# Performance work log

Hardware: AMD Instinct MI355X
Metric: run time of the kernel (lower is better)

The kernel has to match this reference:

```python
import jax, jax.numpy as jnp
import numpy as np

N, IN_C, HID, OUT_C = 50000, 128, 256, 40
L, G = 4, 2
GC = HID // G  # 128 channels per group
E = 600000
EPS = 1e-5


def _ln(h, g, b):
    mu = jnp.mean(h, axis=-1, keepdims=True)
    var = jnp.mean((h - mu) ** 2, axis=-1, keepdims=True)
    return (h - mu) * jax.lax.rsqrt(var + EPS) * g + b


def setup_inputs() -> dict:
    key = jax.random.key(0)
    ks = jax.random.split(key, 16)
    s = lambda k, shape, sc=0.05: jax.random.normal(k, shape, dtype=jnp.float32) * sc
    return {
        "x": jax.random.normal(ks[0], (N, IN_C), dtype=jnp.float32),
        "edge_index": jax.random.randint(ks[1], (2, E), 0, N, dtype=jnp.int64),
        "edge_weight": jax.random.uniform(ks[2], (E,), dtype=jnp.float32),
        "lin1_w": s(ks[3], (IN_C, HID)),
        "lin1_b": jnp.zeros((HID,), jnp.float32),
        "lin2_w": s(ks[4], (HID, OUT_C)),
        "lin2_b": jnp.zeros((OUT_C,), jnp.float32),
        "norm_g": jnp.ones((L, G, GC), jnp.float32),   # per-block LayerNorm gamma
        "norm_b": jnp.zeros((L, G, GC), jnp.float32),  # per-block LayerNorm beta
        "conv_w": s(ks[5], (L, G, GC, GC)),            # per-block GCNConv weight
        "conv_b": jnp.zeros((L, G, GC), jnp.float32),  # per-block GCNConv bias
        "fnorm_g": jnp.ones((HID,), jnp.float32),
        "fnorm_b": jnp.zeros((HID,), jnp.float32),
    }


def reference(x, edge_index, edge_weight, lin1_w, lin1_b, lin2_w, lin2_b,
              norm_g, norm_b, conv_w, conv_b, fnorm_g, fnorm_b):
    src, dst = edge_index[0], edge_index[1]
    h = x @ lin1_w + lin1_b  # [N, HID]
    for l in range(L):
        xs = jnp.split(h, G, axis=-1)  # G x [N, GC]
        ys = []
        y_in = xs[-1]  # GroupAddRev coupling: y_i = x_i + F_i(y_{i-1}), y_{-1} = x_{G-1}
        for g in range(G):
            # GNNBlock: LayerNorm -> ReLU -> GCNConv(normalize=False)
            z = jax.nn.relu(_ln(y_in, norm_g[l, g], norm_b[l, g]))
            z = z @ conv_w[l, g]                       # GCNConv linear
            msg = edge_weight[:, None] * z[src]        # [E, GC]
            agg = jax.ops.segment_sum(msg, dst, num_segments=N) + conv_b[l, g]
            y_in = xs[g] + agg
            ys.append(y_in)
        h = jnp.concatenate(ys, axis=-1)
    h = jax.nn.relu(_ln(h, fnorm_g, fnorm_b))
    return h @ lin2_w + lin2_b  # [N, OUT_C]
```

## Files before the change

### kernel.cpp

```cpp
#include <hip/hip_runtime.h>
#include <stdint.h>

#define NN    50000
#define INC   128
#define HIDC  256
#define OUTC  40
#define GCH   128
#define NL    4
#define NG    2
#define NEDGE 600000
#define EPSV  1e-5f

typedef __bf16 bf16x8 __attribute__((ext_vector_type(8)));
typedef float  f32x4  __attribute__((ext_vector_type(4)));
typedef unsigned short u16x4 __attribute__((ext_vector_type(4)));
typedef unsigned short u16x8 __attribute__((ext_vector_type(8)));

__device__ __forceinline__ float bf2f(unsigned short u) {
    union { float f; unsigned int i; } v;
    v.i = ((unsigned int)u) << 16;
    return v.f;
}
__device__ __forceinline__ unsigned short f2bf(float f) {
    union { float f; unsigned int i; } v;
    v.f = f;
    unsigned int u = v.i;
    u += 0x7FFFu + ((u >> 16) & 1u);
    return (unsigned short)(u >> 16);
}
__device__ __forceinline__ float ldf(const void* p, int is_f32, long long i) {
    if (is_f32) return ((const float*)p)[i];
    return bf2f(((const unsigned short*)p)[i]);
}
__device__ __forceinline__ void gload_lds16(const void* g, void* l) {
    __builtin_amdgcn_global_load_lds(
        (const __attribute__((address_space(1))) unsigned int*)g,
        (__attribute__((address_space(3))) unsigned int*)l,
        16, 0, 0);
}

__global__ void k_marker(void* out, float val, int n) {
    int i = blockIdx.x * 256 + threadIdx.x;
    if (i < n) ((unsigned short*)out)[i] = f2bf(val);
}

__global__ void k_detect(const int* ei, const unsigned short* xprobe,
                         int* flags, int* deg) {
    int t = threadIdx.x;
    int gid = blockIdx.x * 256 + t;
    if (gid < NN) deg[gid] = 0;
    if (blockIdx.x == 0) {
        __shared__ int hi_or, wild_cnt;
        if (t == 0) { hi_or = 0; wild_cnt = 0; }
        __syncthreads();
        int acc = 0;
        for (int i = 0; i < 8; i++) acc |= ei[2 * (t + i * 256) + 1];
        if (acc) atomicOr(&hi_or, 1);
        int wild = 0;
        for (int i = 0; i < 2; i++) {
            unsigned short u = xprobe[t + i * 256];
            int e = (u >> 7) & 0xFF;
            if (e <= 0x30 || e >= 0xC0) wild++;
        }
        atomicAdd(&wild_cnt, wild);
        __syncthreads();
        if (t == 0) {
            flags[0] = hi_or ? 0 : 1;
            flags[1] = (wild_cnt > 32) ? 1 : 0;
        }
    }
}

#define CVT_W1  32768
#define CVT_CW  131072
#define CVT_W2  12288
#define CVT_TOT (CVT_W1 + CVT_CW + CVT_W2)

__global__ void k_convert(const void* w1, const void* cw, const void* w2,
                          const void* b1, const void* ng, const void* nb, const void* cb,
                          const void* fg, const void* fb, const void* b2,
                          const int* flags,
                          unsigned short* w1t, unsigned short* cwt, unsigned short* w2t,
                          float* b1f, float* ngf, float* nbf, float* cbf,
                          float* fgf, float* fbf, float* b2f) {
    int t = threadIdx.x;
    int f32 = flags[1];
    if (blockIdx.x == gridDim.x - 1) {
        b1f[t] = ldf(b1, f32, t);
        fgf[t] = ldf(fg, f32, t);
        fbf[t] = ldf(fb, f32, t);
        if (t < 48) b2f[t] = (t < OUTC) ? ldf(b2, f32, t) : 0.0f;
        for (int i = 0; i < 4; i++) {
            int j = t + i * 256;
            ngf[j] = ldf(ng, f32, j);
            nbf[j] = ldf(nb, f32, j);
            cbf[j] = ldf(cb, f32, j);
        }
        return;
    }
    long long j = (long long)blockIdx.x * 256 + t;
    if (j >= CVT_TOT) return;
    if (j < CVT_W1) {
        int n = (int)(j >> 7), k = (int)(j & 127);
        w1t[n * 128 + (k ^ ((n & 7) << 3))] = f2bf(ldf(w1, f32, (long long)k * HIDC + n));
    } else if (j < CVT_W1 + CVT_CW) {
        long long jj = j - CVT_W1;
        int lg = (int)(jj >> 14);
        int rem = (int)(jj & 16383);
        int n = rem >> 7, k = rem & 127;
        cwt[lg * 16384 + n * 128 + (k ^ ((n & 7) << 3))] =
            f2bf(ldf(cw, f32, (long long)lg * GCH * GCH + (long long)k * GCH + n));
    } else {
        long long jj = j - (CVT_W1 + CVT_CW);
        int n = (int)(jj >> 8), k = (int)(jj & 255);
        w2t[n * 256 + (k ^ ((n & 7) << 3))] =
            (n < OUTC) ? f2bf(ldf(w2, f32, (long long)k * OUTC + n)) : (unsigned short)0;
    }
}

__global__ void k_count(const int* __restrict__ ei, const int* __restrict__ flags,
                        int* __restrict__ deg) {
    int e = (blockIdx.x * 256 + threadIdx.x) * 2;
    if (e >= NEDGE) return;
    int d0, d1;
    if (flags[0]) {
        int4 v = *(const int4*)(ei + 2 * (NEDGE + e));
        d0 = v.x; d1 = v.z;
    } else {
        int2 v = *(const int2*)(ei + NEDGE + e);
        d0 = v.x; d1 = v.y;
    }
    atomicAdd(&deg[d0], 1);
    if (e + 1 < NEDGE) atomicAdd(&deg[d1], 1);
}

#define SCAN_B 49
__global__ void k_scan_a(const int* __restrict__ deg, int* __restrict__ bsum) {
    __shared__ int part[256];
    int b = blockIdx.x, t = threadIdx.x;
    int base = b * 1024 + t * 4;
    int s = 0;
#pragma unroll
    for (int j = 0; j < 4; j++) {
        int i = base + j;
        if (i < NN) s += deg[i];
    }
    part[t] = s;
    __syncthreads();
    for (int off = 128; off > 0; off >>= 1) {
        if (t < off) part[t] += part[t + off];
        __syncthreads();
    }
    if (t == 0) bsum[b] = part[0];
}

__global__ void k_scan_c(const int* __restrict__ deg, const int* __restrict__ bsum,
                         int* __restrict__ rowptr, int* __restrict__ cursor) {
    __shared__ int part[256];
    __shared__ int bbase;
    int b = blockIdx.x, t = threadIdx.x;
    if (t == 0) { int r = 0; for (int i = 0; i < b; i++) r += bsum[i]; bbase = r; }
    int base = b * 1024 + t * 4;
    int v[4];
    int s = 0;
#pragma unroll
    for (int j = 0; j < 4; j++) {
        int i = base + j;
        v[j] = (i < NN) ? deg[i] : 0;
        s += v[j];
    }
    part[t] = s;
    __syncthreads();
    for (int off = 1; off < 256; off <<= 1) {
        int x = (t >= off) ? part[t - off] : 0;
        __syncthreads();
        part[t] += x;
        __syncthreads();
    }
    int run = bbase + part[t] - s;
#pragma unroll
    for (int j = 0; j < 4; j++) {
        int i = base + j;
        if (i < NN) { rowptr[i] = run; cursor[i] = run; }
        run += v[j];
    }
    if (b == SCAN_B - 1 && t == 255) rowptr[NN] = NEDGE;
}

__global__ void k_fill(const int* __restrict__ ei, const void* __restrict__ ew,
                       const int* __restrict__ flags,
                       int* __restrict__ cursor, unsigned int* __restrict__ epk) {
    int e = (blockIdx.x * 256 + threadIdx.x) * 2;
    if (e >= NEDGE) return;
    int is64 = flags[0];
    int f32 = flags[1];
    int d0, s0, d1 = 0, s1 = 0;
    int has1 = (e + 1 < NEDGE);
    if (is64) {
        d0 = ei[2 * (NEDGE + e)];
        s0 = ei[2 * e];
        if (has1) { d1 = ei[2 * (NEDGE + e) + 2]; s1 = ei[2 * e + 2]; }
    } else {
        d0 = ei[NEDGE + e];
        s0 = ei[e];
        if (has1) { d1 = ei[NEDGE + e + 1]; s1 = ei[e + 1]; }
    }
    int p0 = atomicAdd(&cursor[d0], 1);
    int p1 = has1 ? atomicAdd(&cursor[d1], 1) : 0;
    unsigned int w0 = f2bf(ldf(ew, f32, e));
    epk[p0] = (w0 << 16) | (unsigned int)s0;
    if (has1) {
        unsigned int w1 = f2bf(ldf(ew, f32, e + 1));
        epk[p1] = (w1 << 16) | (unsigned int)s1;
    }
}

__global__ __launch_bounds__(256) void k_first(
    const void* __restrict__ x,
    const unsigned short* __restrict__ w1t,
    const float* __restrict__ b1f,
    const float* __restrict__ ngf, const float* __restrict__ nbf,
    const unsigned short* __restrict__ cw0,
    const int* __restrict__ flags,
    unsigned short* __restrict__ h,
    unsigned short* __restrict__ z0)
{
    __shared__ __align__(16) unsigned short xb[64 * 128];
    __shared__ __align__(16) unsigned short wt[128 * 128];
    int t = threadIdx.x;
    int r0 = blockIdx.x * 64;
    int f32x = flags[1];
    int w = t >> 6, lane = t & 63, quad = lane >> 4, ln = lane & 15;
    const f32x4 zf = {0.f, 0.f, 0.f, 0.f};

#pragma unroll
    for (int i = 0; i < 8; i++) {
        int cb = (i * 256 + t) * 16;
        gload_lds16((const char*)w1t + cb, (char*)wt + cb);
    }
#pragma unroll
    for (int i = 0; i < 4; i++) {
        int chunk = i * 256 + t;
        int row = chunk >> 4, c16 = chunk & 15;
        int grow = r0 + row;
        u16x8 val = {0, 0, 0, 0, 0, 0, 0, 0};
        if (grow < NN) {
            if (f32x) {
                const float* p = (const float*)x + (long long)grow * INC + c16 * 8;
                float4 a = *(const float4*)p;
                float4 c = *(const float4*)(p + 4);
                val[0] = f2bf(a.x); val[1] = f2bf(a.y); val[2] = f2bf(a.z); val[3] = f2bf(a.w);
                val[4] = f2bf(c.x); val[5] = f2bf(c.y); val[6] = f2bf(c.z); val[7] = f2bf(c.w);
            } else {
                val = *(const u16x8*)((const unsigned short*)x + (long long)grow * INC + c16 * 8);
            }
        }
        *(u16x8*)((char*)xb + row * 256 + ((c16 * 16) ^ ((row & 7) << 4))) = val;
    }
    __syncthreads();

    f32x4 acc[2][8];
#pragma unroll
    for (int i = 0; i < 2; i++)
#pragma unroll
        for (int j = 0; j < 8; j++) acc[i][j] = zf;

#pragma unroll
    for (int kk = 0; kk < 4; kk++) {
        int cb = kk * 64 + quad * 16;
        int rA = w * 16 + ln;
        bf16x8 a = *(const bf16x8*)((const char*)xb + rA * 256 + (cb ^ ((rA & 7) << 4)));
#pragma unroll
        for (int nf = 0; nf < 8; nf++) {
            int rB = nf * 16 + ln;
            bf16x8 b = *(const bf16x8*)((const char*)wt + rB * 256 + (cb ^ ((rB & 7) << 4)));
            acc[0][nf] = __builtin_amdgcn_mfma_f32_16x16x32_bf16(a, b, acc[0][nf], 0, 0, 0);
        }
    }
    __syncthreads();
#pragma unroll
    for (int i = 0; i < 8; i++) {
        int cb = (i * 256 + t) * 16;
        gload_lds16((const char*)w1t + 32768 + cb, (char*)wt + cb);
    }
    __syncthreads();
#pragma unroll
    for (int kk = 0; kk < 4; kk++) {
        int cb = kk * 64 + quad * 16;
        int rA = w * 16 + ln;
        bf16x8 a = *(const bf16x8*)((const char*)xb + rA * 256 + (cb ^ ((rA & 7) << 4)));
#pragma unroll
        for (int nf = 0; nf < 8; nf++) {
            int rB = nf * 16 + ln;
            bf16x8 b = *(const bf16x8*)((const char*)wt + rB * 256 + (cb ^ ((rB & 7) << 4)));
            acc[1][nf] = __builtin_amdgcn_mfma_f32_16x16x32_bf16(a, b, acc[1][nf], 0, 0, 0);
        }
    }

    float ga8[8], be8[8], yv[8][4];
#pragma unroll
    for (int nf = 0; nf < 8; nf++) {
        int col = nf * 16 + ln;
        float b0 = b1f[col], b1 = b1f[128 + col];
        ga8[nf] = ngf[col]; be8[nf] = nbf[col];
#pragma unroll
        for (int r4 = 0; r4 < 4; r4++) {
            int row = r0 + w * 16 + quad * 4 + r4;
            unsigned short h0 = f2bf(acc[0][nf][r4] + b0);
            unsigned short h1 = f2bf(acc[1][nf][r4] + b1);
            if (row < NN) {
                h[(long long)row * HIDC + col] = h0;
                h[(long long)row * HIDC + 128 + col] = h1;
            }
            yv[nf][r4] = bf2f(h1);
        }
    }
    __syncthreads();
#pragma unroll
    for (int i = 0; i < 8; i++) {
        int cb = (i * 256 + t) * 16;
        gload_lds16((const char*)cw0 + cb, (char*)wt + cb);
    }
    unsigned short* a_tile = xb;
#pragma unroll
    for (int r4 = 0; r4 < 4; r4++) {
        float s = 0.f, q = 0.f;
#pragma unroll
        for (int nf = 0; nf < 8; nf++) { s += yv[nf][r4]; q += yv[nf][r4] * yv[nf][r4]; }
        s += __shfl_xor(s, 1, 64); s += __shfl_xor(s, 2, 64);
        s += __shfl_xor(s, 4, 64); s += __shfl_xor(s, 8, 64);
        q += __shfl_xor(q, 1, 64); q += __shfl_xor(q, 2, 64);
        q += __shfl_xor(q, 4, 64); q += __shfl_xor(q, 8, 64);
        float mu = s * (1.0f / GCH);
        float var = q * (1.0f / GCH) - mu * mu;
        float rs = rsqrtf(var + EPSV);
        int row = w * 16 + quad * 4 + r4;
#pragma unroll
        for (int nf = 0; nf < 8; nf++) {
            float val = (yv[nf][r4] - mu) * rs * ga8[nf] + be8[nf];
            if (val < 0.f) val = 0.f;
            *(unsigned short*)((char*)a_tile + row * 256 +
                               (((nf * 16 + ln) * 2) ^ ((row & 7) << 4))) = f2bf(val);
        }
    }
    __syncthreads();

    f32x4 acc2[8];
#pragma unroll
    for (int j = 0; j < 8; j++) acc2[j] = zf;
#pragma unroll
    for (int kk = 0; kk < 4; kk++) {
        int cb = kk * 64 + quad * 16;
        int rA = w * 16 + ln;
        bf16x8 a = *(const bf16x8*)((const char*)a_tile + rA * 256 + (cb ^ ((rA & 7) << 4)));
#pragma unroll
        for (int nf = 0; nf < 8; nf++) {
            int rB = nf * 16 + ln;
            bf16x8 b = *(const bf16x8*)((const char*)wt + rB * 256 + (cb ^ ((rB & 7) << 4)));
            acc2[nf] = __builtin_amdgcn_mfma_f32_16x16x32_bf16(a, b, acc2[nf], 0, 0, 0);
        }
    }
#pragma unroll
    for (int nf = 0; nf < 8; nf++) {
        int col = nf * 16 + ln;
#pragma unroll
        for (int r4 = 0; r4 < 4; r4++) {
            int row2 = r0 + w * 16 + quad * 4 + r4;
            if (row2 < NN) z0[(long long)row2 * GCH + col] = f2bf(acc2[nf][r4]);
        }
    }
}

__global__ __launch_bounds__(256) void k_fused(
    const int* __restrict__ rowptr, const unsigned int* __restrict__ epk,
    const unsigned short* __restrict__ zin,
    const float* __restrict__ cb,
    unsigned short* __restrict__ h, int out_half,
    const float* __restrict__ ga, const float* __restrict__ be,
    const unsigned short* __restrict__ cwn,
    unsigned short* __restrict__ zout)
{
    __shared__ __align__(16) unsigned short wt[128 * 128];
    __shared__ __align__(16) unsigned short a_tile[64 * 128];
    int t = threadIdx.x;
    int r0 = blockIdx.x * 64;
    int c8 = (t & 15) << 3;

#pragma unroll
    for (int i = 0; i < 8; i++) {
        int cbyte = (i * 256 + t) * 16;
        gload_lds16((const char*)cwn + cbyte, (char*)wt + cbyte);
    }

#pragma unroll 1
    for (int bt = 0; bt < 4; bt++) {
        int row = bt * 16 + (t >> 4);
        int node = r0 + row;
        if (node < NN) {
            int beg = rowptr[node], end = rowptr[node + 1];
            unsigned short* hp = h + (long long)node * HIDC + out_half * GCH + c8;
            u16x8 hv = *(u16x8*)hp;
            const unsigned short* zb = zin + c8;
            float acc[8];
#pragma unroll
            for (int j = 0; j < 8; j++) acc[j] = 0.f;

            int e = beg;
            for (; e + 7 < end; e += 8) {
                unsigned int pe[8];
                u16x8 v[8];
#pragma unroll
                for (int i = 0; i < 8; i++) pe[i] = epk[e + i];
#pragma unroll
                for (int i = 0; i < 8; i++)
                    v[i] = *(const u16x8*)(zb + (long long)(pe[i] & 0xFFFFu) * GCH);
#pragma unroll
                for (int i = 0; i < 8; i++) {
                    float wv = bf2f((unsigned short)(pe[i] >> 16));
#pragma unroll
                    for (int j = 0; j < 8; j++) acc[j] += wv * bf2f(v[i][j]);
                }
            }
            if (e + 3 < end) {
                unsigned int pe[4];
                u16x8 v[4];
#pragma unroll
                for (int i = 0; i < 4; i++) pe[i] = epk[e + i];
#pragma unroll
                for (int i = 0; i < 4; i++)
                    v[i] = *(const u16x8*)(zb + (long long)(pe[i] & 0xFFFFu) * GCH);
#pragma unroll
                for (int i = 0; i < 4; i++) {
                    float wv = bf2f((unsigned short)(pe[i] >> 16));
#pragma unroll
                    for (int j = 0; j < 8; j++) acc[j] += wv * bf2f(v[i][j]);
                }
                e += 4;
            }
            for (; e < end; e++) {
                unsigned int pe = epk[e];
                float w0 = bf2f((unsigned short)(pe >> 16));
                u16x8 v = *(const u16x8*)(zb + (long long)(pe & 0xFFFFu) * GCH);
#pragma unroll
                for (int j = 0; j < 8; j++) acc[j] += w0 * bf2f(v[j]);
            }

            float y[8]; float sum = 0.f, sq = 0.f;
#pragma unroll
            for (int j = 0; j < 8; j++) {
                float yy = bf2f(hv[j]) + acc[j] + cb[c8 + j];
                unsigned short r = f2bf(yy);
                hv[j] = r;
                y[j] = bf2f(r);
                sum += y[j]; sq += y[j] * y[j];
            }
            *(u16x8*)hp = hv;

            sum += __shfl_xor(sum, 1, 64); sum += __shfl_xor(sum, 2, 64);
            sum += __shfl_xor(sum, 4, 64); sum += __shfl_xor(sum, 8, 64);
            sq  += __shfl_xor(sq, 1, 64);  sq  += __shfl_xor(sq, 2, 64);
            sq  += __shfl_xor(sq, 4, 64);  sq  += __shfl_xor(sq, 8, 64);
            float mu = sum * (1.0f / GCH);
            float var = sq * (1.0f / GCH) - mu * mu;
            float rs = rsqrtf(var + EPSV);
            u16x8 o;
#pragma unroll
            for (int j = 0; j < 8; j++) {
                float val = (y[j] - mu) * rs * ga[c8 + j] + be[c8 + j];
                if (val < 0.f) val = 0.f;
                o[j] = f2bf(val);
            }
            *(u16x8*)((char*)a_tile + row * 256 + ((c8 * 2) ^ ((row & 7) << 4))) = o;
        }
    }
    __syncthreads();

    int w = t >> 6, lane = t & 63, quad = lane >> 4, ln = lane & 15;
    const f32x4 zf = {0.f, 0.f, 0.f, 0.f};
    f32x4 acc2[8];
#pragma unroll
    for (int j = 0; j < 8; j++) acc2[j] = zf;
#pragma unroll
    for (int kk = 0; kk < 4; kk++) {
        int cbyte = kk * 64 + quad * 16;
        int rA = w * 16 + ln;
        bf16x8 a = *(const bf16x8*)((const char*)a_tile + rA * 256 + (cbyte ^ ((rA & 7) << 4)));
#pragma unroll
        for (int nf = 0; nf < 8; nf++) {
            int rB = nf * 16 + ln;
            bf16x8 b = *(const bf16x8*)((const char*)wt + rB * 256 + (cbyte ^ ((rB & 7) << 4)));
            acc2[nf] = __builtin_amdgcn_mfma_f32_16x16x32_bf16(a, b, acc2[nf], 0, 0, 0);
        }
    }
#pragma unroll
    for (int nf = 0; nf < 8; nf++) {
        int col = nf * 16 + ln;
#pragma unroll
        for (int r4 = 0; r4 < 4; r4++) {
            int row2 = r0 + w * 16 + quad * 4 + r4;
            if (row2 < NN) zout[(long long)row2 * GCH + col] = f2bf(acc2[nf][r4]);
        }
    }
}

__global__ __launch_bounds__(256) void k_last(
    const int* __restrict__ rowptr, const unsigned int* __restrict__ epk,
    const unsigned short* __restrict__ zin,
    const float* __restrict__ cb,
    unsigned short* __restrict__ h,
    const float* __restrict__ fgf, const float* __restrict__ fbf,
    const unsigned short* __restrict__ w2t,
    const float* __restrict__ b2f,
    const int* __restrict__ flags,
    void* __restrict__ out)
{
    __shared__ __align__(16) unsigned short a_tile[64 * 256];
    __shared__ __align__(16) unsigned short wt[48 * 256];
    int t = threadIdx.x;
    int r0 = blockIdx.x * 64;
    int c8 = (t & 15) << 3;
    const int out_half = 1;

#pragma unroll
    for (int i = 0; i < 6; i++) {
        int cbyte = (i * 256 + t) * 16;
        gload_lds16((const char*)w2t + cbyte, (char*)wt + cbyte);
    }

#pragma unroll 1
    for (int bt = 0; bt < 4; bt++) {
        int row = bt * 16 + (t >> 4);
        int node = r0 + row;
        if (node < NN) {
            int beg = rowptr[node], end = rowptr[node + 1];
            unsigned short* hp = h + (long long)node * HIDC + out_half * GCH + c8;
            u16x8 hv = *(u16x8*)hp;
            const unsigned short* zb = zin + c8;
            float acc[8];
#pragma unroll
            for (int j = 0; j < 8; j++) acc[j] = 0.f;

            int e = beg;
            for (; e + 3 < end; e += 4) {
                unsigned int pe[4];
                u16x8 v[4];
#pragma unroll
                for (int i = 0; i < 4; i++) pe[i] = epk[e + i];
#pragma unroll
                for (int i = 0; i < 4; i++)
                    v[i] = *(const u16x8*)(zb + (long long)(pe[i] & 0xFFFFu) * GCH);
#pragma unroll
                for (int i = 0; i < 4; i++) {
                    float wv = bf2f((unsigned short)(pe[i] >> 16));
#pragma unroll
                    for (int j = 0; j < 8; j++) acc[j] += wv * bf2f(v[i][j]);
                }
            }
            for (; e < end; e++) {
                unsigned int pe = epk[e];
                float w0 = bf2f((unsigned short)(pe >> 16));
                u16x8 v = *(const u16x8*)(zb + (long long)(pe & 0xFFFFu) * GCH);
#pragma unroll
                for (int j = 0; j < 8; j++) acc[j] += w0 * bf2f(v[j]);
            }

            float y[8]; float sum = 0.f, sq = 0.f;
#pragma unroll
            for (int j = 0; j < 8; j++) {
                float yy = bf2f(hv[j]) + acc[j] + cb[c8 + j];
                unsigned short r = f2bf(yy);
                hv[j] = r;
                y[j] = bf2f(r);
                sum += y[j]; sq += y[j] * y[j];
            }
            *(u16x8*)hp = hv;

            float oy[8];
            u16x8 ov = *(const u16x8*)(h + (long long)node * HIDC + (out_half ^ 1) * GCH + c8);
#pragma unroll
            for (int j = 0; j < 8; j++) {
                oy[j] = bf2f(ov[j]);
                sum += oy[j]; sq += oy[j] * oy[j];
            }
            sum += __shfl_xor(sum, 1, 64); sum += __shfl_xor(sum, 2, 64);
            sum += __shfl_xor(sum, 4, 64); sum += __shfl_xor(sum, 8, 64);
            sq  += __shfl_xor(sq, 1, 64);  sq  += __shfl_xor(sq, 2, 64);
            sq  += __shfl_xor(sq, 4, 64);  sq  += __shfl_xor(sq, 8, 64);
            float mu = sum * (1.0f / HIDC);
            float var = sq * (1.0f / HIDC) - mu * mu;
            float rs = rsqrtf(var + EPSV);

            u16x8 o;
            int cn = out_half * GCH + c8;
#pragma unroll
            for (int j = 0; j < 8; j++) {
                float val = (y[j] - mu) * rs * fgf[cn + j] + fbf[cn + j];
                if (val < 0.f) val = 0.f;
                o[j] = f2bf(val);
            }
            *(u16x8*)((char*)a_tile + row * 512 + ((cn * 2) ^ ((row & 7) << 4))) = o;
            int co = (out_half ^ 1) * GCH + c8;
#pragma unroll
            for (int j = 0; j < 8; j++) {
                float val = (oy[j] - mu) * rs * fgf[co + j] + fbf[co + j];
                if (val < 0.f) val = 0.f;
                o[j] = f2bf(val);
            }
            *(u16x8*)((char*)a_tile + row * 512 + ((co * 2) ^ ((row & 7) << 4))) = o;
        }
    }
    __syncthreads();

    int w = t >> 6, lane = t & 63, quad = lane >> 4, ln = lane & 15;
    const f32x4 zf = {0.f, 0.f, 0.f, 0.f};
    f32x4 acc2[3];
#pragma unroll
    for (int j = 0; j < 3; j++) acc2[j] = zf;
#pragma unroll
    for (int kk = 0; kk < 8; kk++) {
        int cbyte = kk * 64 + quad * 16;
        int row = w * 16 + ln;
        bf16x8 a = *(const bf16x8*)((const char*)a_tile + row * 512 + (cbyte ^ ((row & 7) << 4)));
#pragma unroll
        for (int nf = 0; nf < 3; nf++) {
            int rB = nf * 16 + ln;
            bf16x8 b = *(const bf16x8*)((const char*)wt + rB * 512 + (cbyte ^ ((rB & 7) << 4)));
            acc2[nf] = __builtin_amdgcn_mfma_f32_16x16x32_bf16(a, b, acc2[nf], 0, 0, 0);
        }
    }
    int f32o = flags[1];
#pragma unroll
    for (int nf = 0; nf < 3; nf++) {
        int col = nf * 16 + ln;
        if (col >= OUTC) continue;
        float bias = b2f[col];
#pragma unroll
        for (int r4 = 0; r4 < 4; r4++) {
            int row2 = r0 + w * 16 + quad * 4 + r4;
            if (row2 < NN) {
                float val = acc2[nf][r4] + bias;
                long long o = (long long)row2 * OUTC + col;
                if (f32o) ((float*)out)[o] = val;
                else      ((unsigned short*)out)[o] = f2bf(val);
            }
        }
    }
}

extern "C" void kernel_launch(void* const* d_in, const int* in_sizes, int n_in,
                              void* d_out, int out_size, void* d_ws, size_t ws_size,
                              hipStream_t stream)
{
    const void* x       = d_in[0];
    const int*  ei      = (const int*)d_in[1];
    const void* ew      = d_in[2];
    const void* lin1_w  = d_in[3];
    const void* lin1_b  = d_in[4];
    const void* lin2_w  = d_in[5];
    const void* lin2_b  = d_in[6];
    const void* norm_g  = d_in[7];
    const void* norm_b  = d_in[8];
    const void* conv_w  = d_in[9];
    const void* conv_b  = d_in[10];
    const void* fnorm_g = d_in[11];
    const void* fnorm_b = d_in[12];

    char* ws = (char*)d_ws;
    size_t off = 0;
    auto alloc = [&](size_t bytes) { void* p = (void*)(ws + off); off += (bytes + 255) & ~255ull; return p; };

    unsigned short* h      = (unsigned short*)alloc((size_t)NN * HIDC * 2);
    unsigned short* z0     = (unsigned short*)alloc((size_t)NN * GCH * 2);
    unsigned short* z1     = (unsigned short*)alloc((size_t)NN * GCH * 2);
    unsigned short* w1t    = (unsigned short*)alloc((size_t)CVT_W1 * 2);
    unsigned short* cwt    = (unsigned short*)alloc((size_t)CVT_CW * 2);
    unsigned short* w2t    = (unsigned short*)alloc((size_t)CVT_W2 * 2);
    float*          b1f    = (float*)alloc(256 * 4);
    float*          ngf    = (float*)alloc(1024 * 4);
    float*          nbf    = (float*)alloc(1024 * 4);
    float*          cbf    = (float*)alloc(1024 * 4);
    float*          fgf    = (float*)alloc(256 * 4);
    float*          fbf    = (float*)alloc(256 * 4);
    float*          b2f    = (float*)alloc(48 * 4);
    int*            deg    = (int*)alloc((size_t)NN * 4);
    int*            rowptr = (int*)alloc(((size_t)NN + 1) * 4);
    int*            cursor = (int*)alloc((size_t)NN * 4);
    unsigned int*   epk    = (unsigned int*)alloc((size_t)NEDGE * 4);
    int*            flags  = (int*)alloc(256);
    int*            bsum   = (int*)alloc(SCAN_B * 4);

    if (ws_size < off || n_in < 13) {
        float mv = 100.0f + (float)(ws_size >> 20) + ((n_in < 13) ? 10000.0f : 0.0f);
        k_marker<<<(out_size + 255) / 256, 256, 0, stream>>>(d_out, mv, out_size);
        return;
    }

    k_detect<<<196, 256, 0, stream>>>(ei, (const unsigned short*)x, flags, deg);
    k_convert<<<CVT_TOT / 256 + 1, 256, 0, stream>>>(lin1_w, conv_w, lin2_w,
                                                     lin1_b, norm_g, norm_b, conv_b,
                                                     fnorm_g, fnorm_b, lin2_b, flags,
                                                     w1t, cwt, w2t,
                                                     b1f, ngf, nbf, cbf, fgf, fbf, b2f);
    k_count<<<(NEDGE / 2 + 255) / 256, 256, 0, stream>>>(ei, flags, deg);
    k_scan_a<<<SCAN_B, 256, 0, stream>>>(deg, bsum);
    k_scan_c<<<SCAN_B, 256, 0, stream>>>(deg, bsum, rowptr, cursor);
    k_fill<<<(NEDGE / 2 + 255) / 256, 256, 0, stream>>>(ei, ew, flags, cursor, epk);

    const int GB = (NN + 63) / 64;
    k_first<<<GB, 256, 0, stream>>>(x, w1t, b1f, ngf, nbf, cwt, flags, h, z0);
    for (int lg = 0; lg < NL * NG - 1; lg++) {
        unsigned short* zin  = (lg & 1) ? z1 : z0;
        unsigned short* zout = (lg & 1) ? z0 : z1;
        k_fused<<<GB, 256, 0, stream>>>(rowptr, epk, zin, cbf + lg * GCH, h, lg & 1,
                                        ngf + (lg + 1) * GCH, nbf + (lg + 1) * GCH,
                                        cwt + (size_t)(lg + 1) * 16384, zout);
    }
    k_last<<<GB, 256, 0, stream>>>(rowptr, epk, z1, cbf + 7 * GCH, h,
                                   fgf, fbf, w2t, b2f, flags, d_out);
}
```

Baseline: 578.7 us.

## Halve weight LDS tiles, stage weights in phases, raise occupancy hints

Shrinks the weight staging buffer in k_first and k_fused to 64x128 and loads weights in quarter or half chunks with extra barriers between phases. Adds launch_bounds minimum of 5 blocks per SM. k_last drops its LDS weight copy and reads W2 directly from global memory, and unrolls the edge gather loop by 8. The smaller LDS footprint is meant to allow more resident blocks to hide gather latency, at the cost of more synchronisation, possible register pressure from the occupancy hint, and uncached global reads of W2.

```diff
diff --git a/kernel.cpp b/kernel.cpp
--- a/kernel.cpp
+++ b/kernel.cpp
@@ -31,6 +31,9 @@
 __device__ __forceinline__ float ldf(const void* p, int is_f32, long long i) {
     if (is_f32) return ((const float*)p)[i];
     return bf2f(((const unsigned short*)p)[i]);
+}
+__device__ __forceinline__ bf16x8 ld8(const unsigned short* p) {
+    return *(const bf16x8*)p;
 }
 __device__ __forceinline__ void gload_lds16(const void* g, void* l) {
     __builtin_amdgcn_global_load_lds(
@@ -215,7 +218,7 @@
     }
 }
 
-__global__ __launch_bounds__(256) void k_first(
+__global__ __launch_bounds__(256, 5) void k_first(
     const void* __restrict__ x,
     const unsigned short* __restrict__ w1t,
     const float* __restrict__ b1f,
@@ -226,7 +229,7 @@
     unsigned short* __restrict__ z0)
 {
     __shared__ __align__(16) unsigned short xb[64 * 128];
-    __shared__ __align__(16) unsigned short wt[128 * 128];
+    __shared__ __align__(16) unsigned short wt[64 * 128];
     int t = threadIdx.x;
     int r0 = blockIdx.x * 64;
     int f32x = flags[1];
@@ -234,7 +237,7 @@
     const f32x4 zf = {0.f, 0.f, 0.f, 0.f};
 
 #pragma unroll
-    for (int i = 0; i < 8; i++) {
+    for (int i = 0; i < 4; i++) {
         int cb = (i * 256 + t) * 16;
         gload_lds16((const char*)w1t + cb, (char*)wt + cb);
     }
@@ -266,35 +269,36 @@
         for (int j = 0; j < 8; j++) acc[i][j] = zf;
 
 #pragma unroll
-    for (int kk = 0; kk < 4; kk++) {
-        int cb = kk * 64 + quad * 16;
-        int rA = w * 16 + ln;
-        bf16x8 a = *(const bf16x8*)((const char*)xb + rA * 256 + (cb ^ ((rA & 7) << 4)));
-#pragma unroll
-        for (int nf = 0; nf < 8; nf++) {
-            int rB = nf * 16 + ln;
-            bf16x8 b = *(const bf16x8*)((const char*)wt + rB * 256 + (cb ^ ((rB & 7) << 4)));
-            acc[0][nf] = __builtin_amdgcn_mfma_f32_16x16x32_bf16(a, b, acc[0][nf], 0, 0, 0);
-        }
-    }
-    __syncthreads();
-#pragma unroll
-    for (int i = 0; i < 8; i++) {
+    for (int ph = 0; ph < 4; ph++) {
+        int nh = ph >> 1, s = ph & 1;
+#pragma unroll
+        for (int kk = 0; kk < 4; kk++) {
+            int cb = kk * 64 + quad * 16;
+            int rA = w * 16 + ln;
+            bf16x8 a = *(const bf16x8*)((const char*)xb + rA * 256 + (cb ^ ((rA & 7) << 4)));
+#pragma unroll
+            for (int nfl = 0; nfl < 4; nfl++) {
+                int rB = nfl * 16 + ln;
+                bf16x8 b = *(const bf16x8*)((const char*)wt + rB * 256 + (cb ^ ((rB & 7) << 4)));
+                acc[nh][s * 4 + nfl] =
+                    __builtin_amdgcn_mfma_f32_16x16x32_bf16(a, b, acc[nh][s * 4 + nfl], 0, 0, 0);
+            }
+        }
+        __syncthreads();
+        if (ph < 3) {
+#pragma unroll
+            for (int i = 0; i < 4; i++) {
+                int cb = (i * 256 + t) * 16;
+                gload_lds16((const char*)w1t + (ph + 1) * 16384 + cb, (char*)wt + cb);
+            }
+            __syncthreads();
+        }
+    }
+
+#pragma unroll
+    for (int i = 0; i < 4; i++) {
         int cb = (i * 256 + t) * 16;
-        gload_lds16((const char*)w1t + 32768 + cb, (char*)wt + cb);
-    }
-    __syncthreads();
-#pragma unroll
-    for (int kk = 0; kk < 4; kk++) {
-        int cb = kk * 64 + quad * 16;
-        int rA = w * 16 + ln;
-        bf16x8 a = *(const bf16x8*)((const char*)xb + rA * 256 + (cb ^ ((rA & 7) << 4)));
-#pragma unroll
-        for (int nf = 0; nf < 8; nf++) {
-            int rB = nf * 16 + ln;
-            bf16x8 b = *(const bf16x8*)((const char*)wt + rB * 256 + (cb ^ ((rB & 7) << 4)));
-            acc[1][nf] = __builtin_amdgcn_mfma_f32_16x16x32_bf16(a, b, acc[1][nf], 0, 0, 0);
-        }
+        gload_lds16((const char*)cw0 + cb, (char*)wt + cb);
     }
 
     float ga8[8], be8[8], yv[8][4];
@@ -314,12 +318,6 @@
             }
             yv[nf][r4] = bf2f(h1);
         }
-    }
-    __syncthreads();
-#pragma unroll
-    for (int i = 0; i < 8; i++) {
-        int cb = (i * 256 + t) * 16;
-        gload_lds16((const char*)cw0 + cb, (char*)wt + cb);
     }
     unsigned short* a_tile = xb;
 #pragma unroll
@@ -349,15 +347,28 @@
 #pragma unroll
     for (int j = 0; j < 8; j++) acc2[j] = zf;
 #pragma unroll
-    for (int kk = 0; kk < 4; kk++) {
-        int cb = kk * 64 + quad * 16;
-        int rA = w * 16 + ln;
-        bf16x8 a = *(const bf16x8*)((const char*)a_tile + rA * 256 + (cb ^ ((rA & 7) << 4)));
-#pragma unroll
-        for (int nf = 0; nf < 8; nf++) {
-            int rB = nf * 16 + ln;
-            bf16x8 b = *(const bf16x8*)((const char*)wt + rB * 256 + (cb ^ ((rB & 7) << 4)));
-            acc2[nf] = __builtin_amdgcn_mfma_f32_16x16x32_bf16(a, b, acc2[nf], 0, 0, 0);
+    for (int s = 0; s < 2; s++) {
+#pragma unroll
+        for (int kk = 0; kk < 4; kk++) {
+            int cb = kk * 64 + quad * 16;
+            int rA = w * 16 + ln;
+            bf16x8 a = *(const bf16x8*)((const char*)a_tile + rA * 256 + (cb ^ ((rA & 7) << 4)));
+#pragma unroll
+            for (int nfl = 0; nfl < 4; nfl++) {
+                int rB = nfl * 16 + ln;
+                bf16x8 b = *(const bf16x8*)((const char*)wt + rB * 256 + (cb ^ ((rB & 7) << 4)));
+                acc2[s * 4 + nfl] =
+                    __builtin_amdgcn_mfma_f32_16x16x32_bf16(a, b, acc2[s * 4 + nfl], 0, 0, 0);
+            }
+        }
+        if (s == 0) {
+            __syncthreads();
+#pragma unroll
+            for (int i = 0; i < 4; i++) {
+                int cb = (i * 256 + t) * 16;
+                gload_lds16((const char*)cw0 + 16384 + cb, (char*)wt + cb);
+            }
+            __syncthreads();
         }
     }
 #pragma unroll
@@ -371,7 +382,7 @@
     }
 }
 
-__global__ __launch_bounds__(256) void k_fused(
+__global__ __launch_bounds__(256, 5) void k_fused(
     const int* __restrict__ rowptr, const unsigned int* __restrict__ epk,
     const unsigned short* __restrict__ zin,
     const float* __restrict__ cb,
@@ -380,14 +391,14 @@
     const unsigned short* __restrict__ cwn,
     unsigned short* __restrict__ zout)
 {
-    __shared__ __align__(16) unsigned short wt[128 * 128];
+    __shared__ __align__(16) unsigned short wt[64 * 128];
     __shared__ __align__(16) unsigned short a_tile[64 * 128];
     int t = threadIdx.x;
     int r0 = blockIdx.x * 64;
     int c8 = (t & 15) << 3;
 
 #pragma unroll
-    for (int i = 0; i < 8; i++) {
+    for (int i = 0; i < 4; i++) {
         int cbyte = (i * 256 + t) * 16;
         gload_lds16((const char*)cwn + cbyte, (char*)wt + cbyte);
     }
@@ -481,15 +492,28 @@
 #pragma unroll
     for (int j = 0; j < 8; j++) acc2[j] = zf;
 #pragma unroll
-    for (int kk = 0; kk < 4; kk++) {
-        int cbyte = kk * 64 + quad * 16;
-        int rA = w * 16 + ln;
-        bf16x8 a = *(const bf16x8*)((const char*)a_tile + rA * 256 + (cbyte ^ ((rA & 7) << 4)));
-#pragma unroll
-        for (int nf = 0; nf < 8; nf++) {
-            int rB = nf * 16 + ln;
-            bf16x8 b = *(const bf16x8*)((const char*)wt + rB * 256 + (cbyte ^ ((rB & 7) << 4)));
-            acc2[nf] = __builtin_amdgcn_mfma_f32_16x16x32_bf16(a, b, acc2[nf], 0, 0, 0);
+    for (int s = 0; s < 2; s++) {
+#pragma unroll
+        for (int kk = 0; kk < 4; kk++) {
+            int cbyte = kk * 64 + quad * 16;
+            int rA = w * 16 + ln;
+            bf16x8 a = *(const bf16x8*)((const char*)a_tile + rA * 256 + (cbyte ^ ((rA & 7) << 4)));
+#pragma unroll
+            for (int nfl = 0; nfl < 4; nfl++) {
+                int rB = nfl * 16 + ln;
+                bf16x8 b = *(const bf16x8*)((const char*)wt + rB * 256 + (cbyte ^ ((rB & 7) << 4)));
+                acc2[s * 4 + nfl] =
+                    __builtin_amdgcn_mfma_f32_16x16x32_bf16(a, b, acc2[s * 4 + nfl], 0, 0, 0);
+            }
+        }
+        if (s == 0) {
+            __syncthreads();
+#pragma unroll
+            for (int i = 0; i < 4; i++) {
+                int cbyte = (i * 256 + t) * 16;
+                gload_lds16((const char*)cwn + 16384 + cbyte, (char*)wt + cbyte);
+            }
+            __syncthreads();
         }
     }
 #pragma unroll
@@ -503,7 +527,7 @@
     }
 }
 
-__global__ __launch_bounds__(256) void k_last(
+__global__ __launch_bounds__(256, 5) void k_last(
     const int* __restrict__ rowptr, const unsigned int* __restrict__ epk,
     const unsigned short* __restrict__ zin,
     const float* __restrict__ cb,
@@ -515,17 +539,10 @@
     void* __restrict__ out)
 {
     __shared__ __align__(16) unsigned short a_tile[64 * 256];
-    __shared__ __align__(16) unsigned short wt[48 * 256];
     int t = threadIdx.x;
     int r0 = blockIdx.x * 64;
     int c8 = (t & 15) << 3;
     const int out_half = 1;
-
-#pragma unroll
-    for (int i = 0; i < 6; i++) {
-        int cbyte = (i * 256 + t) * 16;
-        gload_lds16((const char*)w2t + cbyte, (char*)wt + cbyte);
-    }
 
 #pragma unroll 1
     for (int bt = 0; bt < 4; bt++) {
@@ -541,7 +558,22 @@
             for (int j = 0; j < 8; j++) acc[j] = 0.f;
 
             int e = beg;
-            for (; e + 3 < end; e += 4) {
+            for (; e + 7 < end; e += 8) {
+                unsigned int pe[8];
+                u16x8 v[8];
+#pragma unroll
+                for (int i = 0; i < 8; i++) pe[i] = epk[e + i];
+#pragma unroll
+                for (int i = 0; i < 8; i++)
+                    v[i] = *(const u16x8*)(zb + (long long)(pe[i] & 0xFFFFu) * GCH);
+#pragma unroll
+                for (int i = 0; i < 8; i++) {
+                    float wv = bf2f((unsigned short)(pe[i] >> 16));
+#pragma unroll
+                    for (int j = 0; j < 8; j++) acc[j] += wv * bf2f(v[i][j]);
+                }
+            }
+            if (e + 3 < end) {
                 unsigned int pe[4];
                 u16x8 v[4];
 #pragma unroll
@@ -555,6 +587,7 @@
 #pragma unroll
                     for (int j = 0; j < 8; j++) acc[j] += wv * bf2f(v[i][j]);
                 }
+                e += 4;
             }
             for (; e < end; e++) {
                 unsigned int pe = epk[e];
@@ -619,12 +652,13 @@
 #pragma unroll
     for (int kk = 0; kk < 8; kk++) {
         int cbyte = kk * 64 + quad * 16;
+        int ko = kk * 32 + quad * 8;
         int row = w * 16 + ln;
         bf16x8 a = *(const bf16x8*)((const char*)a_tile + row * 512 + (cbyte ^ ((row & 7) << 4)));
 #pragma unroll
         for (int nf = 0; nf < 3; nf++) {
             int rB = nf * 16 + ln;
-            bf16x8 b = *(const bf16x8*)((const char*)wt + rB * 512 + (cbyte ^ ((rB & 7) << 4)));
+            bf16x8 b = ld8(w2t + rB * 256 + (ko ^ ((rB & 7) << 3)));
             acc2[nf] = __builtin_amdgcn_mfma_f32_16x16x32_bf16(a, b, acc2[nf], 0, 0, 0);
         }
     }
```

Measured after the change: 464.6 us (median of 2 runs). 19.7% less time.
